# Kernel optimization log

Measured on AMD Instinct MI355X. Metric: run time of the kernel, lower is better.

## Reference

```python
import jax, jax.numpy as jnp
import numpy as np

D_MODEL = 256
N_HEADS = 8
N_LEVELS = 4
N_POINTS = 4
SHAPES = [(128, 128), (64, 64), (32, 32), (16, 16)]  # (H, W) per level


def _query_hw(Lq):
    h = int(Lq ** 0.5)
    w = Lq // h
    if h * w != Lq:
        facs = [(i, Lq // i) for i in range(1, int(Lq ** 0.5) + 1) if Lq % i == 0]
        h, w = min(facs, key=lambda t: abs(t[0] - t[1]))
    return h, w


def _grid_sample(img, grid):
    # img: [B, D, H, W]; grid: [B, Lq, P, 2] in [-1,1] (x, y)
    # bilinear, padding_mode='zeros', align_corners=False
    B, D, H, W = img.shape
    gx, gy = grid[..., 0], grid[..., 1]
    x = ((gx + 1.0) * W - 1.0) * 0.5
    y = ((gy + 1.0) * H - 1.0) * 0.5
    x0 = jnp.floor(x)
    y0 = jnp.floor(y)
    wx1 = x - x0
    wy1 = y - y0
    wx0 = 1.0 - wx1
    wy0 = 1.0 - wy1
    x0i = x0.astype(jnp.int32)
    y0i = y0.astype(jnp.int32)
    x1i = x0i + 1
    y1i = y0i + 1
    img_flat = img.reshape(B, D, H * W)

    def gather(yi, xi):
        valid = (xi >= 0) & (xi < W) & (yi >= 0) & (yi < H)
        idx = jnp.clip(yi, 0, H - 1) * W + jnp.clip(xi, 0, W - 1)  # [B,Lq,P]
        v = jnp.take_along_axis(img_flat, idx.reshape(B, 1, -1), axis=2)
        v = v.reshape(B, D, *yi.shape[1:])  # [B,D,Lq,P]
        return v * valid[:, None].astype(img.dtype)

    return (gather(y0i, x0i) * (wy0 * wx0)[:, None]
            + gather(y0i, x1i) * (wy0 * wx1)[:, None]
            + gather(y1i, x0i) * (wy1 * wx0)[:, None]
            + gather(y1i, x1i) * (wy1 * wx1)[:, None])


def _forward(query, input_flatten, spatial_shapes,
             W_off, b_off, W_attn, b_attn, W_val, b_val, W_out, b_out):
    N, Lq, C = query.shape
    M, L, P = N_HEADS, N_LEVELS, N_POINTS
    D = C // M
    shapes = np.asarray(spatial_shapes)  # static

    value = (input_flatten @ W_val + b_val).reshape(N, -1, M, D)
    off = (query @ W_off + b_off).reshape(N, Lq, M, L, P, 2)
    attn = jax.nn.softmax((query @ W_attn + b_attn).reshape(N, Lq, M, L * P), axis=-1)
    attn = attn.reshape(N, Lq, M, L, P)

    # normalized reference grid derived from Len_q (2D branch)
    qh, qw = _query_hw(Lq)
    ry, rx = jnp.meshgrid(jnp.linspace(0.5, qh - 0.5, qh) / qh,
                          jnp.linspace(0.5, qw - 0.5, qw) / qw, indexing='ij')
    ref = jnp.stack([rx.reshape(-1), ry.reshape(-1)], axis=-1)  # [Lq, 2] (x,y)
    norm = jnp.asarray(np.stack([shapes[:, 1], shapes[:, 0]], -1), jnp.float32)  # [L,2]=(W,H)
    loc = ref[None, :, None, None, None, :] + off / norm[None, None, None, :, None, :]
    grids = 2.0 * loc - 1.0  # [N,Lq,M,L,P,2]

    starts = np.concatenate([[0], np.cumsum(shapes[:, 0] * shapes[:, 1])])
    sampled = []
    for l in range(L):
        H, W = int(shapes[l, 0]), int(shapes[l, 1])
        v = value[:, starts[l]:starts[l + 1]]            # [N, H*W, M, D]
        v = v.transpose(0, 2, 3, 1).reshape(N * M, D, H, W)
        g = grids[:, :, :, l].transpose(0, 2, 1, 3, 4).reshape(N * M, Lq, P, 2)
        sampled.append(_grid_sample(v, g))               # [NM, D, Lq, P]

    vals = jnp.stack(sampled, axis=-2)                   # [NM, D, Lq, L, P]
    # faithful to original: values flattened (P, L)-major, weights (L, P)-major
    vals = vals.transpose(0, 1, 2, 4, 3).reshape(N * M, D, Lq, P * L)
    w = attn.transpose(0, 2, 1, 3, 4).reshape(N * M, 1, Lq, L * P)
    out = (vals * w).sum(-1).reshape(N, M * D, Lq).transpose(0, 2, 1)  # [N,Lq,C]
    return out @ W_out + b_out


def setup_inputs():
    key = jax.random.key(0)
    ks = jax.random.split(key, 12)
    N, Lq, C = 2, 16384, D_MODEL
    M, L, P = N_HEADS, N_LEVELS, N_POINTS
    Lin = sum(h * w for h, w in SHAPES)
    s = 0.02
    # sampling_offsets bias: original directional grid init
    thetas = np.arange(M, dtype=np.float32) * (2.0 * np.pi / M)
    gi = np.stack([np.cos(thetas), np.sin(thetas)], -1)
    gi = gi / np.abs(gi).max(-1, keepdims=True)
    gi = np.tile(gi.reshape(M, 1, 1, 2), (1, L, P, 1))
    for i in range(P):
        gi[:, :, i, :] *= (i + 1)
    inp = {
        'query': jax.random.normal(ks[0], (N, Lq, C), jnp.float32),
        'reference_points': jax.random.uniform(ks[1], (N, Lq, L, 2), jnp.float32),
        'input_flatten': jax.random.normal(ks[2], (N, Lin, C), jnp.float32),
        'spatial_shapes': jnp.array(SHAPES, jnp.int32),
        'level_start_index': jnp.array(np.concatenate([[0], np.cumsum([h * w for h, w in SHAPES[:-1]])]), jnp.int32),
        'W_off': jax.random.normal(ks[3], (C, M * L * P * 2), jnp.float32) * s,
        'b_off': jnp.asarray(gi.reshape(-1), jnp.float32),
        'W_attn': jax.random.normal(ks[4], (C, M * L * P), jnp.float32) * s,
        'b_attn': jnp.zeros((M * L * P,), jnp.float32),
        'W_val': jax.random.normal(ks[5], (C, C), jnp.float32) * (1.0 / np.sqrt(C)),
        'b_val': jnp.zeros((C,), jnp.float32),
        'W_out': jax.random.normal(ks[6], (C, C), jnp.float32) * (1.0 / np.sqrt(C)),
        'b_out': jnp.zeros((C,), jnp.float32),
    }
    return inp


def reference(query, reference_points, input_flatten, spatial_shapes, level_start_index,
              W_off, b_off, W_attn, b_attn, W_val, b_val, W_out, b_out):
    assert reference_points.shape[-1] == 2
    return _forward(query, input_flatten, spatial_shapes,
                    W_off, b_off, W_attn, b_attn, W_val, b_val, W_out, b_out)
```

## Files before the change

### kernel.cpp

```cpp
#include <hip/hip_runtime.h>
#include <math.h>

#define NB   2
#define LQ   16384
#define CDIM 256
#define MH   8
#define DH   32
#define LIN  21760
#define NPIX (NB * LIN)

typedef __attribute__((ext_vector_type(8))) _Float16 f16x8;
typedef __attribute__((ext_vector_type(4))) _Float16 f16x4;
typedef __attribute__((ext_vector_type(4))) float    f32x4;

__device__ __forceinline__ void async16(const void* g, void* l) {
    __builtin_amdgcn_global_load_lds(
        (const __attribute__((address_space(1))) void*)g,
        (__attribute__((address_space(3))) void*)l,
        16, 0, 0);
}

__global__ __launch_bounds__(256) void tsplit_all_kernel(
    const float* __restrict__ Wv, const float* __restrict__ Wo,
    const float* __restrict__ Wf, const float* __restrict__ Wa,
    _Float16* __restrict__ Wvt, _Float16* __restrict__ Wot, _Float16* __restrict__ Wct)
{
    const int i = blockIdx.x * 256 + threadIdx.x;
    const int r = i >> 8;
    const int kk = i & 255;
    if (r < 256) {
        Wvt[r * 256 + kk] = (_Float16)Wv[kk * 256 + r];
    } else if (r < 512) {
        const int n = r - 256;
        Wot[n * 256 + kk] = (_Float16)Wo[kk * 256 + n];
    } else if (r < 768) {
        const int n = r - 512;
        Wct[n * 256 + kk] = (_Float16)Wf[kk * 256 + n];
    } else {
        const int n = r - 768;
        Wct[(256 + n) * 256 + kk] = (_Float16)Wa[kk * 128 + n];
    }
}


template <int OUT_MODE>
__device__ __forceinline__ void gemm_epilogue(
    f32x4 (&acc)[2][8], int bm, int bn, int wave, int quad, int l16,
    const float* bias0, const float* bias1, void* C0, void* C1, int N, int N0)
{
    void* Cb; const float* bb; int ldc, coff;
    if (bn < N0) { Cb = C0; bb = bias0; ldc = N0;     coff = 0;  }
    else         { Cb = C1; bb = bias1; ldc = N - N0; coff = N0; }
    #pragma unroll
    for (int cidx = 0; cidx < 8; ++cidx) {
        const int col = bn + cidx * 16 + quad * 4 - coff;
        const float4 bia = *(const float4*)&bb[col];
        #pragma unroll
        for (int r = 0; r < 2; ++r) {
            const int rr = bm + wave * 32 + r * 16 + l16;
            float4 v;
            v.x = acc[r][cidx][0] + bia.x;
            v.y = acc[r][cidx][1] + bia.y;
            v.z = acc[r][cidx][2] + bia.z;
            v.w = acc[r][cidx][3] + bia.w;
            if (OUT_MODE == 0) {
                *(float4*)&((float*)Cb)[(size_t)rr * ldc + col] = v;
            } else {
                f16x4 h;
                h[0] = (_Float16)v.x; h[1] = (_Float16)v.y;
                h[2] = (_Float16)v.z; h[3] = (_Float16)v.w;
                *(f16x4*)&((_Float16*)Cb)[((size_t)(col >> 5) * NPIX + rr) * 32 + (col & 31)] = h;
            }
        }
    }
}

__device__ __forceinline__ void stage_B(const _Float16* __restrict__ Bt, int bn,
                                        _Float16* Bsh, int tid)
{
    #pragma unroll
    for (int j = 0; j < 16; ++j) {
        const int s = tid + 256 * j;
        const int row = s >> 5, phys = s & 31;
        const int cl = phys ^ (row & 7);
        async16(Bt + (size_t)(bn + row) * 256 + cl * 8, Bsh + s * 8);
    }
}

__device__ __forceinline__ void mfma_step(const _Float16* Bsh, const f16x8 (&ah)[2],
                                          int t, int quad, int l16, f32x4 (&acc)[2][8])
{
    #pragma unroll
    for (int half = 0; half < 2; ++half) {
        f16x8 bh[4];
        #pragma unroll
        for (int c = 0; c < 4; ++c) {
            const int brow = half * 64 + c * 16 + l16;
            const int pb = (t * 4 + quad) ^ (brow & 7);
            bh[c] = *(const f16x8*)&Bsh[brow * 256 + pb * 8];
        }
        #pragma unroll
        for (int r = 0; r < 2; ++r)
            #pragma unroll
            for (int c = 0; c < 4; ++c)
                acc[r][half * 4 + c] = __builtin_amdgcn_mfma_f32_16x16x32_f16(
                    bh[c], ah[r], acc[r][half * 4 + c], 0, 0, 0);
    }
}

__device__ __forceinline__ void core_f16(
    const _Float16* __restrict__ A, const _Float16* __restrict__ Bt,
    int bm, int bn, _Float16* Ash, _Float16* Bsh, f32x4 (&acc)[2][8])
{
    const int tid = threadIdx.x;
    const int wave = tid >> 6, lane = tid & 63;
    const int quad = lane >> 4, l16 = lane & 15;
    stage_B(Bt, bn, Bsh, tid);
    #pragma unroll
    for (int j = 0; j < 16; ++j) {
        const int s = tid + 256 * j;
        const int row = s >> 5, phys = s & 31;
        const int cl = phys ^ (row & 7);
        async16(A + (size_t)(bm + row) * 256 + cl * 8, Ash + s * 8);
    }
    __syncthreads();
    #pragma unroll
    for (int t = 0; t < 8; ++t) {
        f16x8 ah[2];
        #pragma unroll
        for (int r = 0; r < 2; ++r) {
            const int arow = wave * 32 + r * 16 + l16;
            const int pa = (t * 4 + quad) ^ (arow & 7);
            ah[r] = *(const f16x8*)&Ash[arow * 256 + pa * 8];
        }
        mfma_step(Bsh, ah, t, quad, l16, acc);
    }
}

__device__ __forceinline__ void core_f32(
    const float* __restrict__ A, const _Float16* __restrict__ Bt,
    int bm, int bn, float* AshF, _Float16* Bsh, f32x4 (&acc)[2][8])
{
    const int tid = threadIdx.x;
    const int wave = tid >> 6, lane = tid & 63;
    const int quad = lane >> 4, l16 = lane & 15;
    stage_B(Bt, bn, Bsh, tid);
    #pragma unroll
    for (int h = 0; h < 2; ++h) {
        #pragma unroll
        for (int j = 0; j < 16; ++j) {
            const int s = tid + 256 * j;
            const int row = s >> 5, phys = s & 31;
            const int cl = phys ^ (row & 7);
            async16(A + (size_t)(bm + row) * 256 + h * 128 + cl * 4, AshF + s * 4);
        }
        __syncthreads();
        #pragma unroll
        for (int tt = 0; tt < 4; ++tt) {
            const int t = h * 4 + tt;
            f16x8 ah[2];
            #pragma unroll
            for (int r = 0; r < 2; ++r) {
                const int arow = wave * 32 + r * 16 + l16;
                const int cl0 = tt * 8 + quad * 2;
                const int p0 = cl0       ^ (arow & 7);
                const int p1 = (cl0 + 1) ^ (arow & 7);
                const f32x4 a0 = *(const f32x4*)&AshF[arow * 128 + p0 * 4];
                const f32x4 a1 = *(const f32x4*)&AshF[arow * 128 + p1 * 4];
                f16x8 hh;
                hh[0] = (_Float16)a0[0]; hh[1] = (_Float16)a0[1];
                hh[2] = (_Float16)a0[2]; hh[3] = (_Float16)a0[3];
                hh[4] = (_Float16)a1[0]; hh[5] = (_Float16)a1[1];
                hh[6] = (_Float16)a1[2]; hh[7] = (_Float16)a1[3];
                ah[r] = hh;
            }
            mfma_step(Bsh, ah, t, quad, l16, acc);
        }
        if (h == 0) __syncthreads();
    }
}

__global__ __launch_bounds__(256) void gemm12_fullk(
    const float* __restrict__ IF, const float* __restrict__ Q,
    const _Float16* __restrict__ Wvt, const _Float16* __restrict__ Wct,
    const float* __restrict__ b_val, const float* __restrict__ b_off,
    const float* __restrict__ b_attn,
    _Float16* __restrict__ value16, float* __restrict__ offbuf, float* __restrict__ attnbuf)
{
    __shared__ __align__(16) float    AshF[128 * 128];
    __shared__ __align__(16) _Float16 Bsh[128 * 256];
    f32x4 acc[2][8] = {};
    const int tid = threadIdx.x;
    const int wave = tid >> 6, lane = tid & 63;
    const int quad = lane >> 4, l16 = lane & 15;
    const int bid = blockIdx.x;

    if (bid < 680) {
        const int bm = (bid >> 1) * 128, bn = (bid & 1) * 128;
        core_f32(IF, Wvt, bm, bn, AshF, Bsh, acc);
        gemm_epilogue<2>(acc, bm, bn, wave, quad, l16,
                         b_val, b_val, value16, value16, 256, 256);
    } else {
        const int r = bid - 680;
        const int bm = (r / 3) * 128, bn = (r % 3) * 128;
        core_f32(Q, Wct, bm, bn, AshF, Bsh, acc);
        gemm_epilogue<0>(acc, bm, bn, wave, quad, l16,
                         b_off, b_attn, offbuf, attnbuf, 384, 256);
    }
}

__global__ __launch_bounds__(256) void gemm3_fullk(
    const _Float16* __restrict__ A, const _Float16* __restrict__ Wot,
    const float* __restrict__ b_out, float* __restrict__ out)
{
    __shared__ __align__(16) _Float16 Ash[128 * 256];
    __shared__ __align__(16) _Float16 Bsh[128 * 256];
    f32x4 acc[2][8] = {};
    const int tid = threadIdx.x;
    const int wave = tid >> 6, lane = tid & 63;
    const int quad = lane >> 4, l16 = lane & 15;
    const int bm = blockIdx.y * 128, bn = blockIdx.x * 128;
    core_f16(A, Wot, bm, bn, Ash, Bsh, acc);
    gemm_epilogue<0>(acc, bm, bn, wave, quad, l16,
                     b_out, b_out, out, out, 256, 256);
}

__global__ __launch_bounds__(256) void sample_kernel_v10(
    const _Float16* __restrict__ value,
    const float* __restrict__ off,
    const float* __restrict__ attn,
    _Float16* __restrict__ outv)
{
    __shared__ __align__(16) int4   ivt[128][8];
    __shared__ __align__(16) float4 wvt[128][8];

    const int tid = threadIdx.x;
    const int qbase = blockIdx.x * 8;

    #pragma unroll
    for (int j = 0; j < 4; ++j) {
        const int t  = tid + 256 * j;
        const int q  = t >> 7;
        const int m  = (t >> 4) & 7;
        const int pt = t & 15;
        const int l  = pt >> 2;
        const int p  = pt & 3;
        const int qi = qbase + q;
        const int lq = qi & (LQ - 1);
        const int n  = qi >> 14;

        const int Hl = 128 >> l;
        const int STARTS[4] = {0, 16384, 20480, 21504};

        const float2 oxy = *(const float2*)&off[(size_t)qi * 256 + m * 32 + pt * 2];

        const float logit = attn[(size_t)qi * 128 + m * 16 + p * 4 + l];
        float mx = logit;
        #pragma unroll
        for (int d = 1; d < 16; d <<= 1) mx = fmaxf(mx, __shfl_xor(mx, d, 16));
        const float e = __expf(logit - mx);
        float sm = e;
        #pragma unroll
        for (int d = 1; d < 16; d <<= 1) sm += __shfl_xor(sm, d, 16);
        const float w = e / sm;

        const float refx = ((lq & 127) + 0.5f) * (1.0f / 128.0f);
        const float refy = ((lq >> 7)  + 0.5f) * (1.0f / 128.0f);

        const float x = refx * (float)Hl + oxy.x - 0.5f;
        const float y = refy * (float)Hl + oxy.y - 0.5f;
        const float x0f = floorf(x), y0f = floorf(y);
        const int x0 = (int)x0f, y0 = (int)y0f;
        const int x1 = x0 + 1,  y1 = y0 + 1;
        const float fx = x - x0f, fy = y - y0f;
        const float gx = 1.f - fx, gy = 1.f - fy;

        const float vx0 = (x0 >= 0 && x0 < Hl) ? 1.f : 0.f;
        const float vx1 = (x1 >= 0 && x1 < Hl) ? 1.f : 0.f;
        const float vy0 = (y0 >= 0 && y0 < Hl) ? 1.f : 0.f;
        const float vy1 = (y1 >= 0 && y1 < Hl) ? 1.f : 0.f;

        const int x0c = min(max(x0, 0), Hl - 1);
        const int x1c = min(max(x1, 0), Hl - 1);
        const int y0c = min(max(y0, 0), Hl - 1);
        const int y1c = min(max(y1, 0), Hl - 1);

        const int baseb = m * (NPIX * 64) + (n * LIN + STARTS[l]) * 64;
        const int i00 = baseb + (y0c * Hl + x0c) * 64;
        const int i01 = baseb + (y0c * Hl + x1c) * 64;
        const int i10 = baseb + (y1c * Hl + x0c) * 64;
        const int i11 = baseb + (y1c * Hl + x1c) * 64;

        float4 wv;
        wv.x = w * gy * gx * vy0 * vx0;
        wv.y = w * gy * fx * vy0 * vx1;
        wv.z = w * fy * gx * vy1 * vx0;
        wv.w = w * fy * fx * vy1 * vx1;

        const int cc = m ^ (pt & 7);
        int4 iv = {i00, i01, i10, i11};
        ivt[q * 16 + pt][cc] = iv;
        wvt[q * 16 + pt][cc] = wv;
    }
    __syncthreads();

    const int q  = tid >> 5;
    const int m  = (tid >> 2) & 7;
    const int d8 = tid & 3;
    const int qi = qbase + q;
    const unsigned dd = (unsigned)(d8 * 16);
    const char* vp = (const char*)value;

    f32x4 accL = {0.f, 0.f, 0.f, 0.f};
    f32x4 accH = {0.f, 0.f, 0.f, 0.f};
    #pragma unroll
    for (int pt = 0; pt < 16; ++pt) {
        const int cc = m ^ (pt & 7);
        const int4  iv = ivt[q * 16 + pt][cc];
        const float4 wv = wvt[q * 16 + pt][cc];
        const f16x8 v00 = *(const f16x8*)(vp + ((unsigned)iv.x + dd));
        const f16x8 v01 = *(const f16x8*)(vp + ((unsigned)iv.y + dd));
        const f16x8 v10 = *(const f16x8*)(vp + ((unsigned)iv.z + dd));
        const f16x8 v11 = *(const f16x8*)(vp + ((unsigned)iv.w + dd));
        f32x4 l00 = {(float)v00[0], (float)v00[1], (float)v00[2], (float)v00[3]};
        f32x4 h00 = {(float)v00[4], (float)v00[5], (float)v00[6], (float)v00[7]};
        f32x4 l01 = {(float)v01[0], (float)v01[1], (float)v01[2], (float)v01[3]};
        f32x4 h01 = {(float)v01[4], (float)v01[5], (float)v01[6], (float)v01[7]};
        f32x4 l10 = {(float)v10[0], (float)v10[1], (float)v10[2], (float)v10[3]};
        f32x4 h10 = {(float)v10[4], (float)v10[5], (float)v10[6], (float)v10[7]};
        f32x4 l11 = {(float)v11[0], (float)v11[1], (float)v11[2], (float)v11[3]};
        f32x4 h11 = {(float)v11[4], (float)v11[5], (float)v11[6], (float)v11[7]};
        accL += wv.x * l00 + wv.y * l01 + wv.z * l10 + wv.w * l11;
        accH += wv.x * h00 + wv.y * h01 + wv.z * h10 + wv.w * h11;
    }

    f16x8 o;
    o[0] = (_Float16)accL[0]; o[1] = (_Float16)accL[1];
    o[2] = (_Float16)accL[2]; o[3] = (_Float16)accL[3];
    o[4] = (_Float16)accH[0]; o[5] = (_Float16)accH[1];
    o[6] = (_Float16)accH[2]; o[7] = (_Float16)accH[3];
    *(f16x8*)&outv[(size_t)qi * 256 + m * 32 + d8 * 8] = o;
}

extern "C" void kernel_launch(void* const* d_in, const int* in_sizes, int n_in,
                              void* d_out, int out_size, void* d_ws, size_t ws_size,
                              hipStream_t stream)
{
    const float* query         = (const float*)d_in[0];
    const float* input_flatten = (const float*)d_in[2];
    const float* W_off  = (const float*)d_in[5];
    const float* b_off  = (const float*)d_in[6];
    const float* W_attn = (const float*)d_in[7];
    const float* b_attn = (const float*)d_in[8];
    const float* W_val  = (const float*)d_in[9];
    const float* b_val  = (const float*)d_in[10];
    const float* W_out  = (const float*)d_in[11];
    const float* b_out  = (const float*)d_in[12];
    float* out = (float*)d_out;

    char* w = (char*)d_ws;
    _Float16* Sf16 = (_Float16*)w;
    _Float16* value16 = (_Float16*)(w + 23068672);
    float*    attnbuf = (float*)(w + 67633152);
    _Float16* Wvt = (_Float16*)(w + 84410368);
    _Float16* Wot = Wvt + 65536;
    _Float16* Wct = Wot + 65536;
    float* offbuf = out;

    dim3 blk(256);

    tsplit_all_kernel<<<896, blk, 0, stream>>>(W_val, W_out, W_off, W_attn, Wvt, Wot, Wct);

    gemm12_fullk<<<1448, blk, 0, stream>>>(
        input_flatten, query, Wvt, Wct, b_val, b_off, b_attn,
        value16, offbuf, attnbuf);

    sample_kernel_v10<<<4096, blk, 0, stream>>>(value16, offbuf, attnbuf, Sf16);

    gemm3_fullk<<<dim3(2, 256), blk, 0, stream>>>(Sf16, Wot, b_out, out);
}
```

Baseline: 237.3 us.

## Halve GEMM LDS footprint with two-phase K staging, f16 A conversion, XCD swizzle

The GEMM kernels now stage K in two 128-wide phases instead of holding the full K=256 tile. In the f32-input GEMM, A is converted to f16 in registers before the LDS write. This cuts shared memory per block from 96KB/128KB to 64KB, so more blocks can be resident per CU, and removes the repeated f32-to-f16 conversions inside the MFMA loop. Block IDs are remapped with an XCD swizzle so that neighbouring tiles land on the same chiplet for L2 reuse. In exchange there is an extra barrier per phase, and A goes through a synchronous register load rather than an async LDS load.

```diff
diff --git a/kernel.cpp b/kernel.cpp
--- a/kernel.cpp
+++ b/kernel.cpp
@@ -18,6 +18,10 @@
         (const __attribute__((address_space(1))) void*)g,
         (__attribute__((address_space(3))) void*)l,
         16, 0, 0);
+}
+
+__device__ __forceinline__ int xcd_swizzle(int b, int nwg) {
+    return (b & 7) * (nwg >> 3) + (b >> 3);
 }
 
 __global__ __launch_bounds__(256) void tsplit_all_kernel(
@@ -42,6 +46,103 @@
     }
 }
 
+
+__device__ __forceinline__ void stage_f16_half(
+    const _Float16* __restrict__ Src, int brow0, int ph, _Float16* Dsh, int tid)
+{
+    #pragma unroll
+    for (int j = 0; j < 8; ++j) {
+        const int s = tid + 256 * j;
+        const int row = s >> 4, ch = s & 15;
+        const int cl = ch ^ (row & 7);
+        async16(Src + (size_t)(brow0 + row) * 256 + ph * 128 + cl * 8, Dsh + s * 8);
+    }
+}
+
+__device__ __forceinline__ void mfma_phase(
+    const _Float16* Ash, const _Float16* Bsh, int wave, int quad, int l16,
+    f32x4 (&acc)[2][8])
+{
+    #pragma unroll
+    for (int t = 0; t < 4; ++t) {
+        f16x8 ah[2];
+        #pragma unroll
+        for (int r = 0; r < 2; ++r) {
+            const int arow = wave * 32 + r * 16 + l16;
+            const int pa = (t * 4 + quad) ^ (arow & 7);
+            ah[r] = *(const f16x8*)&Ash[arow * 128 + pa * 8];
+        }
+        #pragma unroll
+        for (int half = 0; half < 2; ++half) {
+            f16x8 bh[4];
+            #pragma unroll
+            for (int c = 0; c < 4; ++c) {
+                const int brow = half * 64 + c * 16 + l16;
+                const int pb = (t * 4 + quad) ^ (brow & 7);
+                bh[c] = *(const f16x8*)&Bsh[brow * 128 + pb * 8];
+            }
+            #pragma unroll
+            for (int r = 0; r < 2; ++r)
+                #pragma unroll
+                for (int c = 0; c < 4; ++c)
+                    acc[r][half * 4 + c] = __builtin_amdgcn_mfma_f32_16x16x32_f16(
+                        bh[c], ah[r], acc[r][half * 4 + c], 0, 0, 0);
+        }
+    }
+}
+
+__device__ __forceinline__ void core_f32_128(
+    const float* __restrict__ A, const _Float16* __restrict__ Bt,
+    int bm, int bn, _Float16* Ash, _Float16* Bsh, f32x4 (&acc)[2][8])
+{
+    const int tid = threadIdx.x;
+    const int wave = tid >> 6, lane = tid & 63;
+    const int quad = lane >> 4, l16 = lane & 15;
+    #pragma unroll
+    for (int ph = 0; ph < 2; ++ph) {
+        if (ph) __syncthreads();
+        float4 r0[8], r1[8];
+        #pragma unroll
+        for (int i = 0; i < 8; ++i) {
+            const int v = tid + 256 * i;
+            const int row = v >> 4, ch = v & 15;
+            const float* src = A + (size_t)(bm + row) * 256 + ph * 128 + ch * 8;
+            r0[i] = *(const float4*)src;
+            r1[i] = *(const float4*)(src + 4);
+        }
+        stage_f16_half(Bt, bn, ph, Bsh, tid);
+        #pragma unroll
+        for (int i = 0; i < 8; ++i) {
+            const int v = tid + 256 * i;
+            const int row = v >> 4, ch = v & 15;
+            f16x8 h;
+            h[0] = (_Float16)r0[i].x; h[1] = (_Float16)r0[i].y;
+            h[2] = (_Float16)r0[i].z; h[3] = (_Float16)r0[i].w;
+            h[4] = (_Float16)r1[i].x; h[5] = (_Float16)r1[i].y;
+            h[6] = (_Float16)r1[i].z; h[7] = (_Float16)r1[i].w;
+            *(f16x8*)&Ash[row * 128 + ((ch ^ (row & 7)) * 8)] = h;
+        }
+        __syncthreads();
+        mfma_phase(Ash, Bsh, wave, quad, l16, acc);
+    }
+}
+
+__device__ __forceinline__ void core_f16_128(
+    const _Float16* __restrict__ A, const _Float16* __restrict__ Bt,
+    int bm, int bn, _Float16* Ash, _Float16* Bsh, f32x4 (&acc)[2][8])
+{
+    const int tid = threadIdx.x;
+    const int wave = tid >> 6, lane = tid & 63;
+    const int quad = lane >> 4, l16 = lane & 15;
+    #pragma unroll
+    for (int ph = 0; ph < 2; ++ph) {
+        if (ph) __syncthreads();
+        stage_f16_half(A, bm, ph, Ash, tid);
+        stage_f16_half(Bt, bn, ph, Bsh, tid);
+        __syncthreads();
+        mfma_phase(Ash, Bsh, wave, quad, l16, acc);
+    }
+}
 
 template <int OUT_MODE>
 __device__ __forceinline__ void gemm_epilogue(
@@ -75,152 +176,48 @@
     }
 }
 
-__device__ __forceinline__ void stage_B(const _Float16* __restrict__ Bt, int bn,
-                                        _Float16* Bsh, int tid)
-{
-    #pragma unroll
-    for (int j = 0; j < 16; ++j) {
-        const int s = tid + 256 * j;
-        const int row = s >> 5, phys = s & 31;
-        const int cl = phys ^ (row & 7);
-        async16(Bt + (size_t)(bn + row) * 256 + cl * 8, Bsh + s * 8);
-    }
-}
-
-__device__ __forceinline__ void mfma_step(const _Float16* Bsh, const f16x8 (&ah)[2],
-                                          int t, int quad, int l16, f32x4 (&acc)[2][8])
-{
-    #pragma unroll
-    for (int half = 0; half < 2; ++half) {
-        f16x8 bh[4];
-        #pragma unroll
-        for (int c = 0; c < 4; ++c) {
-            const int brow = half * 64 + c * 16 + l16;
-            const int pb = (t * 4 + quad) ^ (brow & 7);
-            bh[c] = *(const f16x8*)&Bsh[brow * 256 + pb * 8];
-        }
-        #pragma unroll
-        for (int r = 0; r < 2; ++r)
-            #pragma unroll
-            for (int c = 0; c < 4; ++c)
-                acc[r][half * 4 + c] = __builtin_amdgcn_mfma_f32_16x16x32_f16(
-                    bh[c], ah[r], acc[r][half * 4 + c], 0, 0, 0);
-    }
-}
-
-__device__ __forceinline__ void core_f16(
-    const _Float16* __restrict__ A, const _Float16* __restrict__ Bt,
-    int bm, int bn, _Float16* Ash, _Float16* Bsh, f32x4 (&acc)[2][8])
-{
-    const int tid = threadIdx.x;
-    const int wave = tid >> 6, lane = tid & 63;
-    const int quad = lane >> 4, l16 = lane & 15;
-    stage_B(Bt, bn, Bsh, tid);
-    #pragma unroll
-    for (int j = 0; j < 16; ++j) {
-        const int s = tid + 256 * j;
-        const int row = s >> 5, phys = s & 31;
-        const int cl = phys ^ (row & 7);
-        async16(A + (size_t)(bm + row) * 256 + cl * 8, Ash + s * 8);
-    }
-    __syncthreads();
-    #pragma unroll
-    for (int t = 0; t < 8; ++t) {
-        f16x8 ah[2];
-        #pragma unroll
-        for (int r = 0; r < 2; ++r) {
-            const int arow = wave * 32 + r * 16 + l16;
-            const int pa = (t * 4 + quad) ^ (arow & 7);
-            ah[r] = *(const f16x8*)&Ash[arow * 256 + pa * 8];
-        }
-        mfma_step(Bsh, ah, t, quad, l16, acc);
-    }
-}
-
-__device__ __forceinline__ void core_f32(
-    const float* __restrict__ A, const _Float16* __restrict__ Bt,
-    int bm, int bn, float* AshF, _Float16* Bsh, f32x4 (&acc)[2][8])
-{
-    const int tid = threadIdx.x;
-    const int wave = tid >> 6, lane = tid & 63;
-    const int quad = lane >> 4, l16 = lane & 15;
-    stage_B(Bt, bn, Bsh, tid);
-    #pragma unroll
-    for (int h = 0; h < 2; ++h) {
-        #pragma unroll
-        for (int j = 0; j < 16; ++j) {
-            const int s = tid + 256 * j;
-            const int row = s >> 5, phys = s & 31;
-            const int cl = phys ^ (row & 7);
-            async16(A + (size_t)(bm + row) * 256 + h * 128 + cl * 4, AshF + s * 4);
-        }
-        __syncthreads();
-        #pragma unroll
-        for (int tt = 0; tt < 4; ++tt) {
-            const int t = h * 4 + tt;
-            f16x8 ah[2];
-            #pragma unroll
-            for (int r = 0; r < 2; ++r) {
-                const int arow = wave * 32 + r * 16 + l16;
-                const int cl0 = tt * 8 + quad * 2;
-                const int p0 = cl0       ^ (arow & 7);
-                const int p1 = (cl0 + 1) ^ (arow & 7);
-                const f32x4 a0 = *(const f32x4*)&AshF[arow * 128 + p0 * 4];
-                const f32x4 a1 = *(const f32x4*)&AshF[arow * 128 + p1 * 4];
-                f16x8 hh;
-                hh[0] = (_Float16)a0[0]; hh[1] = (_Float16)a0[1];
-                hh[2] = (_Float16)a0[2]; hh[3] = (_Float16)a0[3];
-                hh[4] = (_Float16)a1[0]; hh[5] = (_Float16)a1[1];
-                hh[6] = (_Float16)a1[2]; hh[7] = (_Float16)a1[3];
-                ah[r] = hh;
-            }
-            mfma_step(Bsh, ah, t, quad, l16, acc);
-        }
-        if (h == 0) __syncthreads();
-    }
-}
-
-__global__ __launch_bounds__(256) void gemm12_fullk(
+__global__ __launch_bounds__(256) void gemm12_v3(
     const float* __restrict__ IF, const float* __restrict__ Q,
     const _Float16* __restrict__ Wvt, const _Float16* __restrict__ Wct,
     const float* __restrict__ b_val, const float* __restrict__ b_off,
     const float* __restrict__ b_attn,
     _Float16* __restrict__ value16, float* __restrict__ offbuf, float* __restrict__ attnbuf)
 {
-    __shared__ __align__(16) float    AshF[128 * 128];
-    __shared__ __align__(16) _Float16 Bsh[128 * 256];
+    __shared__ __align__(16) _Float16 Ash[128 * 128];
+    __shared__ __align__(16) _Float16 Bsh[128 * 128];
     f32x4 acc[2][8] = {};
     const int tid = threadIdx.x;
     const int wave = tid >> 6, lane = tid & 63;
     const int quad = lane >> 4, l16 = lane & 15;
-    const int bid = blockIdx.x;
-
-    if (bid < 680) {
-        const int bm = (bid >> 1) * 128, bn = (bid & 1) * 128;
-        core_f32(IF, Wvt, bm, bn, AshF, Bsh, acc);
+    const int wid = xcd_swizzle(blockIdx.x, 1448);
+
+    if (wid < 680) {
+        const int bm = (wid >> 1) * 128, bn = (wid & 1) * 128;
+        core_f32_128(IF, Wvt, bm, bn, Ash, Bsh, acc);
         gemm_epilogue<2>(acc, bm, bn, wave, quad, l16,
                          b_val, b_val, value16, value16, 256, 256);
     } else {
-        const int r = bid - 680;
+        const int r = wid - 680;
         const int bm = (r / 3) * 128, bn = (r % 3) * 128;
-        core_f32(Q, Wct, bm, bn, AshF, Bsh, acc);
+        core_f32_128(Q, Wct, bm, bn, Ash, Bsh, acc);
         gemm_epilogue<0>(acc, bm, bn, wave, quad, l16,
                          b_off, b_attn, offbuf, attnbuf, 384, 256);
     }
 }
 
-__global__ __launch_bounds__(256) void gemm3_fullk(
+__global__ __launch_bounds__(256) void gemm3_v3(
     const _Float16* __restrict__ A, const _Float16* __restrict__ Wot,
     const float* __restrict__ b_out, float* __restrict__ out)
 {
-    __shared__ __align__(16) _Float16 Ash[128 * 256];
-    __shared__ __align__(16) _Float16 Bsh[128 * 256];
+    __shared__ __align__(16) _Float16 Ash[128 * 128];
+    __shared__ __align__(16) _Float16 Bsh[128 * 128];
     f32x4 acc[2][8] = {};
     const int tid = threadIdx.x;
     const int wave = tid >> 6, lane = tid & 63;
     const int quad = lane >> 4, l16 = lane & 15;
-    const int bm = blockIdx.y * 128, bn = blockIdx.x * 128;
-    core_f16(A, Wot, bm, bn, Ash, Bsh, acc);
+    const int wid = xcd_swizzle(blockIdx.x, 512);
+    const int bm = (wid >> 1) * 128, bn = (wid & 1) * 128;
+    core_f16_128(A, Wot, bm, bn, Ash, Bsh, acc);
     gemm_epilogue<0>(acc, bm, bn, wave, quad, l16,
                      b_out, b_out, out, out, 256, 256);
 }
@@ -371,11 +368,11 @@
 
     tsplit_all_kernel<<<896, blk, 0, stream>>>(W_val, W_out, W_off, W_attn, Wvt, Wot, Wct);
 
-    gemm12_fullk<<<1448, blk, 0, stream>>>(
+    gemm12_v3<<<1448, blk, 0, stream>>>(
         input_flatten, query, Wvt, Wct, b_val, b_off, b_attn,
         value16, offbuf, attnbuf);
 
     sample_kernel_v10<<<4096, blk, 0, stream>>>(value16, offbuf, attnbuf, Sf16);
 
-    gemm3_fullk<<<dim3(2, 256), blk, 0, stream>>>(Sf16, Wot, b_out, out);
-}
+    gemm3_v3<<<512, blk, 0, stream>>>(Sf16, Wot, b_out, out);
+}
```

Result: faster. 225.3 us (-5.0%).
